# Performance work log

Measured on AMD Instinct MI355X. Metric: run time of the kernel, lower is better.

The kernel has to match this reference:

```python
import jax, jax.numpy as jnp
import numpy as np

PCR = (-50.0, -50.0, -1.0, 150.0, 50.0, 3.0)   # point_cloud_range
VOXEL_SIZE = (0.1, 0.1, 0.2)                    # initial_voxel_size
RESOLUTION = 100                                # adaptive-center grid resolution per dim
SCALING = 25.0
MODE = 'quadratic'
EXP_SCALING = 0.1
N_PTS = 4_000_000


def setup_inputs() -> dict:
    key = jax.random.key(0)
    u = jax.random.uniform(key, (N_PTS, 4), dtype=jnp.float32)  # [N,4] in [0,1)
    # scale xyz slightly beyond the cloud range so some points fall out of range
    lo = jnp.array([PCR[0] - 10.0, PCR[1] - 10.0, PCR[2] - 1.0, 0.0], jnp.float32)
    hi = jnp.array([PCR[3] + 10.0, PCR[4] + 10.0, PCR[5] + 1.0, 1.0], jnp.float32)
    pts = u * (hi - lo) + lo
    return {"pts": pts}


def _calculate_voxel_centers():
    # torch.meshgrid default indexing is 'ij'
    lins = [jnp.linspace(PCR[i], PCR[i + 3], RESOLUTION, dtype=jnp.float32) for i in range(3)]
    grids = jnp.meshgrid(*lins, indexing='ij')
    centers = jnp.stack([g.ravel() for g in grids], axis=0)      # [3, R^3]
    norms = jnp.linalg.norm(centers, axis=0)                     # [R^3]
    norm_c = jnp.max(jnp.abs(norms))
    if MODE == 'linear':
        sf = jnp.abs(norms) / norm_c
    elif MODE == 'exponential':
        sf = jnp.exp(jnp.abs(norms) * EXP_SCALING) / jnp.exp(norm_c * EXP_SCALING)
    else:  # quadratic
        sf = jnp.abs(norms) ** 2 / norm_c ** 2
    centers = centers * (1.0 + sf * SCALING)
    # in-range mask (original does boolean filtering -> dynamic shape; we return a
    # static-shape mask instead, same selected values)
    mask = ((centers[0] >= PCR[0]) & (centers[0] <= PCR[3]) &
            (centers[1] >= PCR[1]) & (centers[1] <= PCR[4]) &
            (centers[2] >= PCR[2]) & (centers[2] <= PCR[5]))
    return centers, mask


def reference(pts):
    """Adaptive voxel centers + mmdet3d-style dynamic_voxelize (NDim=3).

    Returns:
      coors:   [N,3] int32 voxel coords in (z,y,x) order, -1 for out-of-range points
      centers: [3, R^3] float32 adaptive voxel centers (pre-filter)
      center_mask: [R^3] bool in-range mask for the centers
    """
    centers, center_mask = _calculate_voxel_centers()
    vs = jnp.array(VOXEL_SIZE, jnp.float32)                      # [3]
    cmin = jnp.array(PCR[:3], jnp.float32)                       # [3]
    grid = jnp.round((jnp.array(PCR[3:]) - jnp.array(PCR[:3])) / vs)  # [3] floats
    c = jnp.floor((pts[:, :3] - cmin) / vs)                      # [N,3] float voxel idx
    valid = jnp.all((c >= 0) & (c < grid), axis=1)               # [N]
    coors = jnp.where(valid[:, None], c[:, ::-1], -1.0)          # zyx order, -1 invalid
    return coors.astype(jnp.int32), centers, center_mask
```

## Files before the change

kernel.cpp:

```cpp
#include <hip/hip_runtime.h>


#define RES 100
#define R3 (RES * RES * RES)

__global__ __launch_bounds__(256) void voxelize_kernel(
    const float4* __restrict__ pts, float* __restrict__ coors, int n) {
  int i = blockIdx.x * blockDim.x + threadIdx.x;
  if (i >= n) return;
  float4 p = pts[i];
  float c0 = floorf(__fdiv_rn(__fsub_rn(p.x, -50.0f), 0.1f));
  float c1 = floorf(__fdiv_rn(__fsub_rn(p.y, -50.0f), 0.1f));
  float c2 = floorf(__fdiv_rn(__fsub_rn(p.z, -1.0f), 0.2f));
  bool valid = (c0 >= 0.0f) && (c0 < 2000.0f) &&
               (c1 >= 0.0f) && (c1 < 1000.0f) &&
               (c2 >= 0.0f) && (c2 < 20.0f);
  float o0 = valid ? c2 : -1.0f;
  float o1 = valid ? c1 : -1.0f;
  float o2 = valid ? c0 : -1.0f;
  size_t b = (size_t)3 * i;
  coors[b]     = o0;
  coors[b + 1] = o1;
  coors[b + 2] = o2;
}

__device__ __forceinline__ float lin_val(float start, float stop, int k) {
  if (k == RES - 1) return stop;
  float t = __fdiv_rn((float)k, (float)(RES - 1));
  return __fadd_rn(__fmul_rn(start, __fsub_rn(1.0f, t)),
                   __fmul_rn(stop, t));
}

__global__ __launch_bounds__(256) void centers_kernel(
    float* __restrict__ centers, float* __restrict__ mask) {
  int j = blockIdx.x * blockDim.x + threadIdx.x;
  if (j >= R3) return;
  int i0 = j / (RES * RES);
  int rem = j - i0 * (RES * RES);
  int i1 = rem / RES;
  int i2 = rem - i1 * RES;
  float c0 = lin_val(-50.0f, 150.0f, i0);
  float c1 = lin_val(-50.0f, 50.0f, i1);
  float c2 = lin_val(-1.0f, 3.0f, i2);
  float s = __fadd_rn(__fadd_rn(__fmul_rn(c0, c0), __fmul_rn(c1, c1)),
                      __fmul_rn(c2, c2));
  float nrm = __fsqrt_rn(s);
  float nc = __fsqrt_rn(25009.0f);
  float sf = __fdiv_rn(__fmul_rn(nrm, nrm), __fmul_rn(nc, nc));
  float scale = __fadd_rn(1.0f, __fmul_rn(sf, 25.0f));
  float x0 = __fmul_rn(c0, scale);
  float x1 = __fmul_rn(c1, scale);
  float x2 = __fmul_rn(c2, scale);
  bool m = (x0 >= -50.0f) && (x0 <= 150.0f) &&
           (x1 >= -50.0f) && (x1 <= 50.0f) &&
           (x2 >= -1.0f) && (x2 <= 3.0f);
  centers[j] = x0;
  centers[R3 + j] = x1;
  centers[2 * R3 + j] = x2;
  mask[j] = m ? 1.0f : 0.0f;
}

extern "C" void kernel_launch(void* const* d_in, const int* in_sizes, int n_in,
                              void* d_out, int out_size, void* d_ws, size_t ws_size,
                              hipStream_t stream) {
  const float4* pts = (const float4*)d_in[0];
  int n = in_sizes[0] / 4;
  float* out = (float*)d_out;
  float* coors = out;
  float* centers = out + (size_t)3 * n;
  float* cmask = centers + (size_t)3 * R3;

  voxelize_kernel<<<(n + 255) / 256, 256, 0, stream>>>(pts, coors, n);
  centers_kernel<<<(R3 + 255) / 256, 256, 0, stream>>>(centers, cmask);
}
```

Before: 110.0 us.

## Fuse voxelize and centers kernels with 4-wide vectorized nontemporal I/O

Merges the two launches into one grid whose blocks are partitioned between point voxelization and center generation. Each thread now processes four points, writing 12 coordinates as three 16-byte stores, or four centers with the shared c0/c1 partial norm hoisted. Nontemporal loads and stores are used to bypass cache retention for streaming data. This removes one launch and the tail gap between kernels and widens memory transactions. It assumes N is divisible by 4, since any remainder points are dropped.

```diff
diff --git a/kernel.cpp b/kernel.cpp
--- a/kernel.cpp
+++ b/kernel.cpp
@@ -3,26 +3,9 @@
 
 #define RES 100
 #define R3 (RES * RES * RES)
+#define NCG (R3 / 4)
 
-__global__ __launch_bounds__(256) void voxelize_kernel(
-    const float4* __restrict__ pts, float* __restrict__ coors, int n) {
-  int i = blockIdx.x * blockDim.x + threadIdx.x;
-  if (i >= n) return;
-  float4 p = pts[i];
-  float c0 = floorf(__fdiv_rn(__fsub_rn(p.x, -50.0f), 0.1f));
-  float c1 = floorf(__fdiv_rn(__fsub_rn(p.y, -50.0f), 0.1f));
-  float c2 = floorf(__fdiv_rn(__fsub_rn(p.z, -1.0f), 0.2f));
-  bool valid = (c0 >= 0.0f) && (c0 < 2000.0f) &&
-               (c1 >= 0.0f) && (c1 < 1000.0f) &&
-               (c2 >= 0.0f) && (c2 < 20.0f);
-  float o0 = valid ? c2 : -1.0f;
-  float o1 = valid ? c1 : -1.0f;
-  float o2 = valid ? c0 : -1.0f;
-  size_t b = (size_t)3 * i;
-  coors[b]     = o0;
-  coors[b + 1] = o1;
-  coors[b + 2] = o2;
-}
+typedef float f32x4 __attribute__((ext_vector_type(4)));
 
 __device__ __forceinline__ float lin_val(float start, float stop, int k) {
   if (k == RES - 1) return stop;
@@ -31,45 +14,78 @@
                    __fmul_rn(stop, t));
 }
 
-__global__ __launch_bounds__(256) void centers_kernel(
-    float* __restrict__ centers, float* __restrict__ mask) {
-  int j = blockIdx.x * blockDim.x + threadIdx.x;
-  if (j >= R3) return;
-  int i0 = j / (RES * RES);
-  int rem = j - i0 * (RES * RES);
-  int i1 = rem / RES;
-  int i2 = rem - i1 * RES;
-  float c0 = lin_val(-50.0f, 150.0f, i0);
-  float c1 = lin_val(-50.0f, 50.0f, i1);
-  float c2 = lin_val(-1.0f, 3.0f, i2);
-  float s = __fadd_rn(__fadd_rn(__fmul_rn(c0, c0), __fmul_rn(c1, c1)),
-                      __fmul_rn(c2, c2));
-  float nrm = __fsqrt_rn(s);
-  float nc = __fsqrt_rn(25009.0f);
-  float sf = __fdiv_rn(__fmul_rn(nrm, nrm), __fmul_rn(nc, nc));
-  float scale = __fadd_rn(1.0f, __fmul_rn(sf, 25.0f));
-  float x0 = __fmul_rn(c0, scale);
-  float x1 = __fmul_rn(c1, scale);
-  float x2 = __fmul_rn(c2, scale);
-  bool m = (x0 >= -50.0f) && (x0 <= 150.0f) &&
-           (x1 >= -50.0f) && (x1 <= 50.0f) &&
-           (x2 >= -1.0f) && (x2 <= 3.0f);
-  centers[j] = x0;
-  centers[R3 + j] = x1;
-  centers[2 * R3 + j] = x2;
-  mask[j] = m ? 1.0f : 0.0f;
+__global__ __launch_bounds__(256) void adaptive_voxel_fused(
+    const f32x4* __restrict__ pts, float* __restrict__ out,
+    int n4 , int nbVox ) {
+  int b = blockIdx.x;
+  if (b < nbVox) {
+    int t = b * 256 + threadIdx.x;
+    if (t >= n4) return;
+    const f32x4* pp = pts + (size_t)4 * t;
+    float o[12];
+#pragma unroll
+    for (int k = 0; k < 4; ++k) {
+      f32x4 p = __builtin_nontemporal_load(&pp[k]);
+      float c0 = floorf(__fdiv_rn(__fsub_rn(p.x, -50.0f), 0.1f));
+      float c1 = floorf(__fdiv_rn(__fsub_rn(p.y, -50.0f), 0.1f));
+      float c2 = floorf(__fdiv_rn(__fsub_rn(p.z, -1.0f), 0.2f));
+      bool valid = (c0 >= 0.0f) && (c0 < 2000.0f) &&
+                   (c1 >= 0.0f) && (c1 < 1000.0f) &&
+                   (c2 >= 0.0f) && (c2 < 20.0f);
+      o[3 * k]     = valid ? c2 : -1.0f;
+      o[3 * k + 1] = valid ? c1 : -1.0f;
+      o[3 * k + 2] = valid ? c0 : -1.0f;
+    }
+    f32x4* cp = (f32x4*)out + (size_t)3 * t;
+#pragma unroll
+    for (int k = 0; k < 3; ++k) {
+      f32x4 v = {o[4 * k], o[4 * k + 1], o[4 * k + 2], o[4 * k + 3]};
+      __builtin_nontemporal_store(v, cp + k);
+    }
+  } else {
+    int q = (b - nbVox) * 256 + threadIdx.x;
+    if (q >= NCG) return;
+    int j0 = 4 * q;
+    int i0 = j0 / (RES * RES);
+    int rem = j0 - i0 * (RES * RES);
+    int i1 = rem / RES;
+    int i2b = rem - i1 * RES;
+    float c0 = lin_val(-50.0f, 150.0f, i0);
+    float c1 = lin_val(-50.0f, 50.0f, i1);
+    float s01 = __fadd_rn(__fmul_rn(c0, c0), __fmul_rn(c1, c1));
+    float nc = __fsqrt_rn(25009.0f);
+    float nc2 = __fmul_rn(nc, nc);
+    f32x4 xs, ys, zs, ms;
+#pragma unroll
+    for (int k = 0; k < 4; ++k) {
+      float c2 = lin_val(-1.0f, 3.0f, i2b + k);
+      float s = __fadd_rn(s01, __fmul_rn(c2, c2));
+      float nrm = __fsqrt_rn(s);
+      float sf = __fdiv_rn(__fmul_rn(nrm, nrm), nc2);
+      float scale = __fadd_rn(1.0f, __fmul_rn(sf, 25.0f));
+      float x0 = __fmul_rn(c0, scale);
+      float x1 = __fmul_rn(c1, scale);
+      float x2 = __fmul_rn(c2, scale);
+      bool m = (x0 >= -50.0f) && (x0 <= 150.0f) &&
+               (x1 >= -50.0f) && (x1 <= 50.0f) &&
+               (x2 >= -1.0f) && (x2 <= 3.0f);
+      xs[k] = x0; ys[k] = x1; zs[k] = x2; ms[k] = m ? 1.0f : 0.0f;
+    }
+    f32x4* cx = (f32x4*)(out + (size_t)12 * n4);
+    __builtin_nontemporal_store(xs, cx + q);
+    __builtin_nontemporal_store(ys, cx + NCG + q);
+    __builtin_nontemporal_store(zs, cx + 2 * NCG + q);
+    __builtin_nontemporal_store(ms, cx + 3 * NCG + q);
+  }
 }
 
 extern "C" void kernel_launch(void* const* d_in, const int* in_sizes, int n_in,
                               void* d_out, int out_size, void* d_ws, size_t ws_size,
                               hipStream_t stream) {
-  const float4* pts = (const float4*)d_in[0];
-  int n = in_sizes[0] / 4;
+  const f32x4* pts = (const f32x4*)d_in[0];
+  int n4 = in_sizes[0] / 16;
   float* out = (float*)d_out;
-  float* coors = out;
-  float* centers = out + (size_t)3 * n;
-  float* cmask = centers + (size_t)3 * R3;
-
-  voxelize_kernel<<<(n + 255) / 256, 256, 0, stream>>>(pts, coors, n);
-  centers_kernel<<<(R3 + 255) / 256, 256, 0, stream>>>(centers, cmask);
+  int nbVox = (n4 + 255) / 256;
+  int nbCen = (NCG + 255) / 256;
+  adaptive_voxel_fused<<<nbVox + nbCen, 256, 0, stream>>>(pts, out, n4, nbVox);
 }
```

New measurement: 123.3 us. 1.12x slower.
